# Optimization experiments

Measured on AMD Instinct MI355X. Metric: run time of the kernel, lower is better.

Reference implementation:

```python
import jax, jax.numpy as jnp
import numpy as np

B, N, NODE, EDGE, H, SK, SV, PK, PV = 1, 512, 256, 128, 8, 16, 16, 4, 4
EPS = 1e-8
SCALAR_SCALE = (3 * SK) ** -0.5          # num_attn_logits=3
POINT_SCALE = (3 * PK * (9.0 / 2.0)) ** -0.5
PAIR_SCALE = 3 ** -0.5


def setup_inputs() -> dict:
    key = jax.random.key(0)
    ks = jax.random.split(key, 16)
    s = 0.02
    return {
        "node": jax.random.normal(ks[0], (B, N, NODE), jnp.float32),
        "edge": jax.random.normal(ks[1], (B, N, N, EDGE), jnp.float32),
        "rotations": jax.random.normal(ks[2], (B, N, 3, 3), jnp.float32),
        "translations": jax.random.normal(ks[3], (B, N, 3), jnp.float32),
        "W_sq": jax.random.normal(ks[4], (NODE, H * SK), jnp.float32) * s,
        "W_sk": jax.random.normal(ks[5], (NODE, H * SK), jnp.float32) * s,
        "W_sv": jax.random.normal(ks[6], (NODE, H * SV), jnp.float32) * s,
        "W_pq": jax.random.normal(ks[7], (NODE, H * PK * 3), jnp.float32) * s,
        "W_pk": jax.random.normal(ks[8], (NODE, H * PK * 3), jnp.float32) * s,
        "W_pv": jax.random.normal(ks[9], (NODE, H * PV * 3), jnp.float32) * s,
        "point_weights": jnp.log(jnp.expm1(jnp.ones((H,), jnp.float32))),  # softplus^-1(1)
        "W_pb": jax.random.normal(ks[10], (EDGE, H), jnp.float32) * s,
        "b_pb": jnp.zeros((H,), jnp.float32),
        "W_out": jax.random.normal(ks[11], (H * (SV + EDGE + PV * 4), NODE), jnp.float32) * s,
        "b_out": jnp.zeros((NODE,), jnp.float32),
    }


def reference(node, edge, rotations, translations, W_sq, W_sk, W_sv, W_pq, W_pk, W_pv,
              point_weights, W_pb, b_pb, W_out, b_out):
    b, n, _ = node.shape
    # scalar q/k/v: (b, n, h, d)
    qs = (node @ W_sq).reshape(b, n, H, SK)
    ks_ = (node @ W_sk).reshape(b, n, H, SK)
    vs = (node @ W_sv).reshape(b, n, H, SV)
    # point q/k/v in local frame: (b, n, h, d, 3) -> rotate + translate into global frame
    t = translations[:, :, None, None, :]  # (b, n, 1, 1, 3)
    qp = jnp.einsum('bnhdc,bnrc->bnhdr', (node @ W_pq).reshape(b, n, H, PK, 3), rotations) + t
    kp = jnp.einsum('bnhdc,bnrc->bnhdr', (node @ W_pk).reshape(b, n, H, PK, 3), rotations) + t
    vp = jnp.einsum('bnhdc,bnrc->bnhdr', (node @ W_pv).reshape(b, n, H, PV, 3), rotations) + t

    # scalar logits (b, h, i, j)
    logits_scalar = jnp.einsum('bihd,bjhd->bhij', qs, ks_) * SCALAR_SCALE
    # pairwise bias (b, h, i, j)
    logits_pair = (jnp.einsum('bijd,dh->bhij', edge, W_pb) + b_pb[None, :, None, None]) * PAIR_SCALE
    # point logits: sum_{d,c} ||q - k||^2 via expansion (avoids (b,i,j,h,d,3) tensor)
    q2 = (qp ** 2).sum((-2, -1)).transpose(0, 2, 1)  # (b, h, i)
    k2 = (kp ** 2).sum((-2, -1)).transpose(0, 2, 1)  # (b, h, j)
    cross = jnp.einsum('bihdc,bjhdc->bhij', qp, kp)
    point_dist = q2[:, :, :, None] + k2[:, :, None, :] - 2.0 * cross  # (b, h, i, j)
    pw = jax.nn.softplus(point_weights)[None, :, None, None]  # (1, h, 1, 1)
    logits_points = -0.5 * (point_dist * pw * POINT_SCALE)

    attn = jax.nn.softmax(logits_scalar + logits_points + logits_pair, axis=-1)  # (b, h, i, j)

    res_scalar = jnp.einsum('bhij,bjhd->bihd', attn, vs).reshape(b, n, H * SV)
    res_pair = jnp.einsum('bhij,bijd->bihd', attn, edge).reshape(b, n, H * EDGE)
    res_pts = jnp.einsum('bhij,bjhdr->bihdr', attn, vp) - t  # back to origin
    res_pts = jnp.einsum('bnhdr,bnrc->bnhdc', res_pts, rotations)  # inverse rotation (R^T)
    res_norm = jnp.sqrt((res_pts ** 2).sum(-1) + EPS)  # (b, n, h, d)

    out = jnp.concatenate([
        res_scalar,
        res_pts.reshape(b, n, H * PV * 3),
        res_norm.reshape(b, n, H * PV),
        res_pair,
    ], axis=-1)
    return out @ W_out + b_out
```

## Files before the change

kernel.cpp:

```cpp
#include <hip/hip_runtime.h>
#include <hip/hip_fp16.h>
#include <math.h>

#define NN 512
#define NODE_D 256
#define EDGE_D 128
#define HN 8

#define SCALAR_SCALE 0.14433756729740643f
#define POINT_SCALE  0.13608276348795434f
#define PAIR_SCALE   0.5773502691896258f

#define OFF_QS   0
#define OFF_KS   65536
#define OFF_VS   131072
#define OFF_VP   196608
#define OFF_QCAT 245760
#define OFF_KCAT 393216
#define OFF_FEAT 540672
#define OFF_PRAW OFF_FEAT
#define OFF_LG16 1196032
#define OFF_OUTP 2244608
#define OFF_PART 2768896

__global__ __launch_bounds__(256) void k_projgemm(
    const float* __restrict__ node,
    const float* __restrict__ Wsq, const float* __restrict__ Wsk, const float* __restrict__ Wsv,
    const float* __restrict__ Wpq, const float* __restrict__ Wpk, const float* __restrict__ Wpv,
    float* __restrict__ ws)
{
  __shared__ float As[32 * 33];
  __shared__ float Bs[32 * 36];
  const int t = threadIdx.x;
  const int it = blockIdx.x;
  const int ct = blockIdx.y;

  const float* W; int ncol, col0; float* dst; int ldd, dcol0;
  if (ct < 12) {
    int a = ct >> 2;
    W = (a == 0) ? Wsq : (a == 1) ? Wsk : Wsv;
    ncol = 128; col0 = (ct & 3) * 32;
    dst = ws + ((a == 0) ? OFF_QS : (a == 1) ? OFF_KS : OFF_VS);
    ldd = 128; dcol0 = col0;
  } else {
    int p = ct - 12;
    int a = p / 3, cc = p % 3;
    W = (a == 0) ? Wpq : (a == 1) ? Wpk : Wpv;
    ncol = 96; col0 = cc * 32;
    dst = ws + OFF_PRAW;
    ldd = 288; dcol0 = a * 96 + cc * 32;
  }

  const int row = t & 31, cb = (t >> 5) * 4;
  float4 acc = {0.f, 0.f, 0.f, 0.f};

  for (int kt = 0; kt < 8; ++kt) {
    __syncthreads();
    #pragma unroll
    for (int q = 0; q < 4; ++q) {
      int f = t + q * 256; int r = f >> 5, c = f & 31;
      As[r * 33 + c] = node[(size_t)(it * 32 + r) * 256 + kt * 32 + c];
      Bs[r * 36 + c] = W[(size_t)(kt * 32 + r) * ncol + col0 + c];
    }
    __syncthreads();
    #pragma unroll
    for (int k = 0; k < 32; ++k) {
      float a = As[row * 33 + k];
      float4 b = *(const float4*)&Bs[k * 36 + cb];
      acc.x += a * b.x; acc.y += a * b.y; acc.z += a * b.z; acc.w += a * b.w;
    }
  }
  *(float4*)&dst[(size_t)(it * 32 + row) * ldd + dcol0 + cb] = acc;
}

__global__ __launch_bounds__(256) void k_rot2(
    const float* __restrict__ rotm, const float* __restrict__ trans,
    const float* __restrict__ pw_in, const float* __restrict__ bpb,
    float* __restrict__ ws)
{
  __shared__ float p_l[4][288];
  __shared__ float r_l[4][288];
  __shared__ float q2_l[4][8];
  __shared__ float k2_l[4][8];
  __shared__ float pw_l[8];
  __shared__ float bpb_l[8];
  const int t = threadIdx.x;
  const int n0 = blockIdx.x * 4;
  const float* praw = ws + OFF_PRAW;
  const float* qs_g = ws + OFF_QS;
  const float* ks_g = ws + OFF_KS;

  if (t < 8) {
    float x = pw_in[t];
    pw_l[t] = 0.5f * POINT_SCALE * logf(1.0f + expf(x));
    bpb_l[t] = bpb[t];
  }
  for (int idx = t; idx < 1152; idx += 256) {
    int row = idx / 288, rem = idx % 288;
    p_l[row][rem] = praw[(size_t)(n0 + row) * 288 + rem];
  }
  __syncthreads();

  for (int idx = t; idx < 1152; idx += 256) {
    int row = idx / 288, rem = idx % 288;
    int a = rem / 96, col = rem % 96;
    int rr = col % 3;
    int n = n0 + row;
    const float* R = rotm + (size_t)(n * 3 + rr) * 3;
    const float* P = &p_l[row][a * 96 + (col - rr)];
    float val = P[0] * R[0] + P[1] * R[1] + P[2] * R[2] + trans[n * 3 + rr];
    r_l[row][a * 96 + col] = val;
    if (a == 2) (ws + OFF_VP)[(size_t)n * 96 + col] = val;
  }
  __syncthreads();

  if (t < 64) {
    int row = t >> 4, rem = t & 15;
    int which = rem >> 3, h = rem & 7;
    const float* src = &r_l[row][which * 96 + h * 12];
    float s = 0.f;
    #pragma unroll
    for (int m = 0; m < 12; ++m) s += src[m] * src[m];
    if (which == 0) q2_l[row][h] = s; else k2_l[row][h] = s;
  }
  __syncthreads();

  for (int idx = t; idx < 2304; idx += 256) {
    int side = idx >= 1152;
    int per = idx - side * 1152;
    int row = per / 288, s = per % 288;
    int h = s / 36, e = s % 36;
    int n = n0 + row;
    float val;
    if (!side) {
      val = (e < 16) ? qs_g[(size_t)n * 128 + h * 16 + e] * SCALAR_SCALE
          : (e < 28) ? 2.0f * pw_l[h] * r_l[row][h * 12 + (e - 16)]
          : (e == 32) ? -pw_l[h]
          : (e == 33) ? (bpb_l[h] * PAIR_SCALE - pw_l[h] * q2_l[row][h])
          : 0.f;
      (ws + OFF_QCAT)[(size_t)n * 288 + s] = val;
    } else {
      val = (e < 16) ? ks_g[(size_t)n * 128 + h * 16 + e]
          : (e < 28) ? r_l[row][96 + h * 12 + (e - 16)]
          : (e == 32) ? k2_l[row][h]
          : (e == 33) ? 1.f
          : 0.f;
      (ws + OFF_KCAT)[(size_t)n * 288 + s] = val;
    }
  }
}

__global__ __launch_bounds__(256) void k_S(
    const float* __restrict__ ws_c, __half* __restrict__ lg16)
{
  __shared__ float4 Qt[32 * 36];
  __shared__ float4 Kt[32 * 37];
  __shared__ __half lgst[32 * 32 * 8];
  const int t = threadIdx.x;
  const int it = blockIdx.x, jt = blockIdx.y;
  const float* Qc = ws_c + OFF_QCAT;
  const float* Kc = ws_c + OFF_KCAT;
  const int ti = t >> 4, tj = t & 15;

  for (int hg = 0; hg < 2; ++hg) {
    __syncthreads();
    for (int f = t; f < 1152; f += 256) {
      int row = f / 36, c = f % 36;
      Qt[row * 36 + c] = *(const float4*)&Qc[(size_t)(it * 32 + row) * 288 + hg * 144 + c * 4];
      Kt[row * 37 + c] = *(const float4*)&Kc[(size_t)(jt * 32 + row) * 288 + hg * 144 + c * 4];
    }
    __syncthreads();

    float acc[2][2][4];
    #pragma unroll
    for (int a = 0; a < 2; ++a)
      #pragma unroll
      for (int b = 0; b < 2; ++b)
        #pragma unroll
        for (int h = 0; h < 4; ++h) acc[a][b][h] = 0.f;

    for (int c = 0; c < 9; ++c) {
      #pragma unroll
      for (int hh = 0; hh < 4; ++hh) {
        float4 q0 = Qt[(2 * ti + 0) * 36 + hh * 9 + c];
        float4 q1 = Qt[(2 * ti + 1) * 36 + hh * 9 + c];
        float4 k0 = Kt[(2 * tj + 0) * 37 + hh * 9 + c];
        float4 k1 = Kt[(2 * tj + 1) * 37 + hh * 9 + c];
        acc[0][0][hh] += q0.x * k0.x + q0.y * k0.y + q0.z * k0.z + q0.w * k0.w;
        acc[0][1][hh] += q0.x * k1.x + q0.y * k1.y + q0.z * k1.z + q0.w * k1.w;
        acc[1][0][hh] += q1.x * k0.x + q1.y * k0.y + q1.z * k0.z + q1.w * k0.w;
        acc[1][1][hh] += q1.x * k1.x + q1.y * k1.y + q1.z * k1.z + q1.w * k1.w;
      }
    }
    #pragma unroll
    for (int a = 0; a < 2; ++a)
      #pragma unroll
      for (int b = 0; b < 2; ++b)
        #pragma unroll
        for (int hh = 0; hh < 4; ++hh)
          lgst[((2 * ti + a) * 32 + (2 * tj + b)) * 8 + hg * 4 + hh] = __float2half(acc[a][b][hh]);
  }
  __syncthreads();

  for (int f = t; f < 1024; f += 256) {
    int il = f >> 5, jl = f & 31;
    float4 v = *(const float4*)&lgst[(il * 32 + jl) * 8];
    *(float4*)&lg16[((size_t)(it * 32 + il) * 512 + jt * 32 + jl) * 8] = v;
  }
}

__global__ __launch_bounds__(256) void k_attnfused2(
    const float* __restrict__ edge, const float* __restrict__ ws_r,
    const __half* __restrict__ lg16, const float* __restrict__ Wpb,
    float* __restrict__ part)
{
  __shared__ float e_l[2][32][132];
  __shared__ float w_t[8][33];
  __shared__ float lg_t[32][9];
  __shared__ float mh[8], sh[8], resc[8];
  __shared__ float vsp[4 * 128];
  __shared__ float vpp[4 * 96];

  const int t = threadIdx.x;
  const int jc = blockIdx.x;
  const int i  = blockIdx.y;
  const int dq = t & 31, jg = t >> 5;
  const int sub = t & 15;
  const int hv = dq >> 2;
  const int hp = (dq < 24) ? (dq / 3) : 0;

  const float* eb  = edge + ((size_t)i * 512 + jc * 256) * 128;
  const float* vsg = ws_r + OFF_VS + (size_t)jc * 256 * 128;
  const float* vpg = ws_r + OFF_VP + (size_t)jc * 256 * 96;
  const __half* lgb = lg16 + ((size_t)i * 512 + jc * 256) * 8;

  float wv[8][8];
  #pragma unroll
  for (int dd = 0; dd < 8; ++dd)
    #pragma unroll
    for (int h = 0; h < 8; ++h)
      wv[dd][h] = Wpb[(size_t)(sub * 8 + dd) * 8 + h] * PAIR_SCALE;

  if (t < 8) { mh[t] = -1e30f; sh[t] = 0.f; }

  float4 accp[8];
  #pragma unroll
  for (int h = 0; h < 8; ++h) accp[h] = {0.f, 0.f, 0.f, 0.f};
  float4 accv = {0.f, 0.f, 0.f, 0.f};
  float4 accw = {0.f, 0.f, 0.f, 0.f};

  #pragma unroll
  for (int p = 0; p < 4; ++p) {
    int f = p * 256 + t, r = f >> 5, g = f & 31;
    *(float4*)&e_l[0][r][g * 4] = *(const float4*)&eb[(size_t)r * 128 + g * 4];
  }
  __syncthreads();

  int cur = 0;
  for (int tile = 0; tile < 8; ++tile) {
    float4 nxt0, nxt1, nxt2, nxt3;
    if (tile < 7) {
      const float* ebn = eb + (size_t)(tile + 1) * 32 * 128;
      { int f = t;           int r = f >> 5, g = f & 31; nxt0 = *(const float4*)&ebn[(size_t)r * 128 + g * 4]; }
      { int f = 256 + t;     int r = f >> 5, g = f & 31; nxt1 = *(const float4*)&ebn[(size_t)r * 128 + g * 4]; }
      { int f = 512 + t;     int r = f >> 5, g = f & 31; nxt2 = *(const float4*)&ebn[(size_t)r * 128 + g * 4]; }
      { int f = 768 + t;     int r = f >> 5, g = f & 31; nxt3 = *(const float4*)&ebn[(size_t)r * 128 + g * 4]; }
    }

    #pragma unroll
    for (int pass = 0; pass < 2; ++pass) {
      const int jrow = (t >> 4) + pass * 16;
      float p8[8] = {0, 0, 0, 0, 0, 0, 0, 0};
      #pragma unroll
      for (int k = 0; k < 2; ++k) {
        float4 e = *(float4*)&e_l[cur][jrow][(sub * 2 + k) * 4];
        #pragma unroll
        for (int h = 0; h < 8; ++h)
          p8[h] += e.x * wv[k * 4 + 0][h] + e.y * wv[k * 4 + 1][h]
                 + e.z * wv[k * 4 + 2][h] + e.w * wv[k * 4 + 3][h];
      }
      #pragma unroll
      for (int m = 1; m <= 8; m <<= 1)
        #pragma unroll
        for (int h = 0; h < 8; ++h) p8[h] += __shfl_xor(p8[h], m);
      if (sub == 0) {
        #pragma unroll
        for (int h = 0; h < 8; ++h) lg_t[jrow][h] = p8[h];
      }
    }
    __syncthreads();

    {
      const int hS = t >> 5, jS = t & 31;
      float x = lg_t[jS][hS]
              + __half2float(lgb[(size_t)(tile * 32 + jS) * 8 + hS]);
      float mt = x;
      #pragma unroll
      for (int s = 16; s; s >>= 1) mt = fmaxf(mt, __shfl_xor(mt, s));
      float mo = mh[hS];
      float mn = fmaxf(mo, mt);
      float w = __expf(x - mn);
      float sw = w;
      #pragma unroll
      for (int s = 16; s; s >>= 1) sw += __shfl_xor(sw, s);
      w_t[hS][jS] = w;
      if (jS == 0) {
        float r = __expf(mo - mn);
        resc[hS] = r;
        mh[hS] = mn;
        sh[hS] = sh[hS] * r + sw;
      }
    }
    __syncthreads();

    {
      #pragma unroll
      for (int h = 0; h < 8; ++h) {
        float r = resc[h];
        accp[h].x *= r; accp[h].y *= r; accp[h].z *= r; accp[h].w *= r;
      }
      {
        float rv = resc[hv];
        accv.x *= rv; accv.y *= rv; accv.z *= rv; accv.w *= rv;
      }
      if (dq < 24) {
        float rp = resc[hp];
        accw.x *= rp; accw.y *= rp; accw.z *= rp; accw.w *= rp;
      }
      #pragma unroll
      for (int jj = 0; jj < 4; ++jj) {
        const int j = jg * 4 + jj;
        float4 e = *(float4*)&e_l[cur][j][dq * 4];
        float wj[8];
        #pragma unroll
        for (int h = 0; h < 8; ++h) wj[h] = w_t[h][j];
        #pragma unroll
        for (int h = 0; h < 8; ++h) {
          accp[h].x += wj[h] * e.x; accp[h].y += wj[h] * e.y;
          accp[h].z += wj[h] * e.z; accp[h].w += wj[h] * e.w;
        }
        const int gj = tile * 32 + j;
        float4 v = *(const float4*)&vsg[(size_t)gj * 128 + dq * 4];
        float wvv = wj[hv];
        accv.x += wvv * v.x; accv.y += wvv * v.y;
        accv.z += wvv * v.z; accv.w += wvv * v.w;
        if (dq < 24) {
          float4 pv = *(const float4*)&vpg[(size_t)gj * 96 + dq * 4];
          float wpp = wj[hp];
          accw.x += wpp * pv.x; accw.y += wpp * pv.y;
          accw.z += wpp * pv.z; accw.w += wpp * pv.w;
        }
      }
    }
    __syncthreads();

    if (tile < 7) {
      { int f = t;       int r = f >> 5, g = f & 31; *(float4*)&e_l[cur ^ 1][r][g * 4] = nxt0; }
      { int f = 256 + t; int r = f >> 5, g = f & 31; *(float4*)&e_l[cur ^ 1][r][g * 4] = nxt1; }
      { int f = 512 + t; int r = f >> 5, g = f & 31; *(float4*)&e_l[cur ^ 1][r][g * 4] = nxt2; }
      { int f = 768 + t; int r = f >> 5, g = f & 31; *(float4*)&e_l[cur ^ 1][r][g * 4] = nxt3; }
      cur ^= 1;
      __syncthreads();
    }
  }

  #pragma unroll
  for (int h = 0; h < 8; ++h) {
    accp[h].x += __shfl_xor(accp[h].x, 32);
    accp[h].y += __shfl_xor(accp[h].y, 32);
    accp[h].z += __shfl_xor(accp[h].z, 32);
    accp[h].w += __shfl_xor(accp[h].w, 32);
  }
  accv.x += __shfl_xor(accv.x, 32); accv.y += __shfl_xor(accv.y, 32);
  accv.z += __shfl_xor(accv.z, 32); accv.w += __shfl_xor(accv.w, 32);
  accw.x += __shfl_xor(accw.x, 32); accw.y += __shfl_xor(accw.y, 32);
  accw.z += __shfl_xor(accw.z, 32); accw.w += __shfl_xor(accw.w, 32);

  const int wid = t >> 6;
  float* pl = (float*)e_l;
  if ((t & 63) < 32) {
    #pragma unroll
    for (int h = 0; h < 8; ++h)
      *(float4*)&pl[(size_t)(wid * 8 + h) * 132 + dq * 4] = accp[h];
    *(float4*)&vsp[wid * 128 + dq * 4] = accv;
    if (dq < 24) *(float4*)&vpp[wid * 96 + dq * 4] = accw;
  }
  __syncthreads();

  float* pp = part + ((size_t)i * 2 + jc) * 1280;
  if (t < 8) { pp[t] = mh[t]; pp[8 + t] = sh[t]; }
  {
    const int h = t >> 5, d4 = (t & 31) * 4;
    float4 s = {0.f, 0.f, 0.f, 0.f};
    #pragma unroll
    for (int q = 0; q < 4; ++q) {
      float4 v = *(float4*)&pl[(size_t)(q * 8 + h) * 132 + d4];
      s.x += v.x; s.y += v.y; s.z += v.z; s.w += v.w;
    }
    *(float4*)&pp[16 + h * 128 + d4] = s;
  }
  if (t < 128)
    pp[1040 + t] = vsp[t] + vsp[128 + t] + vsp[256 + t] + vsp[384 + t];
  if (t < 96)
    pp[1168 + t] = vpp[t] + vpp[96 + t] + vpp[192 + t] + vpp[288 + t];
}

__global__ __launch_bounds__(256) void k_amerge(
    const float* __restrict__ part, const float* __restrict__ rotm,
    const float* __restrict__ trans, float* __restrict__ feat)
{
  __shared__ float r0s[8], r1s[8], lis[8];
  __shared__ float op_l[96], rp_l[96];
  const int t = threadIdx.x, i = blockIdx.x;
  const float* p0 = part + (size_t)i * 2560;
  const float* p1 = p0 + 1280;

  if (t < 8) {
    float m0 = p0[t], m1 = p1[t];
    float M = fmaxf(m0, m1);
    float r0 = __expf(m0 - M), r1 = __expf(m1 - M);
    float S = p0[8 + t] * r0 + p1[8 + t] * r1;
    r0s[t] = r0; r1s[t] = r1; lis[t] = 1.0f / S;
  }
  __syncthreads();

  float* frow = feat + (size_t)i * 1280;
  {
    const int h = t >> 5, d4 = (t & 31) * 4;
    float4 a = *(const float4*)&p0[16 + h * 128 + d4];
    float4 b = *(const float4*)&p1[16 + h * 128 + d4];
    float r0 = r0s[h], r1 = r1s[h], li = lis[h];
    float4 o;
    o.x = (a.x * r0 + b.x * r1) * li;
    o.y = (a.y * r0 + b.y * r1) * li;
    o.z = (a.z * r0 + b.z * r1) * li;
    o.w = (a.w * r0 + b.w * r1) * li;
    *(float4*)&frow[256 + h * 128 + d4] = o;
  }
  if (t < 128) {
    int h = t >> 4;
    frow[t] = (p0[1040 + t] * r0s[h] + p1[1040 + t] * r1s[h]) * lis[h];
  }
  if (t < 96) {
    int h = t / 12;
    op_l[t] = (p0[1168 + t] * r0s[h] + p1[1168 + t] * r1s[h]) * lis[h]
            - trans[i * 3 + (t % 3)];
  }
  __syncthreads();

  if (t < 96) {
    int c = t % 3, base = t - c;
    const float* R = rotm + (size_t)i * 9;
    float val = op_l[base] * R[c] + op_l[base + 1] * R[3 + c] + op_l[base + 2] * R[6 + c];
    rp_l[t] = val;
    frow[128 + t] = val;
  }
  __syncthreads();
  if (t < 32) {
    float x = rp_l[t * 3], y = rp_l[t * 3 + 1], z = rp_l[t * 3 + 2];
    frow[224 + t] = sqrtf(x * x + y * y + z * z + 1e-8f);
  }
}

__global__ __launch_bounds__(256) void k_outp(
    const float* __restrict__ feat, const float* __restrict__ Wout,
    float* __restrict__ ws)
{
  __shared__ float As[32 * 33];
  __shared__ float Bs[32 * 36];
  const int t = threadIdx.x;
  const int it = blockIdx.x, ot = blockIdx.y, z = blockIdx.z;
  const int row = t & 31, cb = (t >> 5) * 4;
  float4 acc = {0.f, 0.f, 0.f, 0.f};

  for (int kk = 0; kk < 10; ++kk) {
    int kt = z * 10 + kk;
    __syncthreads();
    #pragma unroll
    for (int q = 0; q < 4; ++q) {
      int f = t + q * 256; int r = f >> 5, c = f & 31;
      As[r * 33 + c] = feat[(size_t)(it * 32 + r) * 1280 + kt * 32 + c];
      Bs[r * 36 + c] = Wout[(size_t)(kt * 32 + r) * 256 + ot * 32 + c];
    }
    __syncthreads();
    #pragma unroll
    for (int k = 0; k < 32; ++k) {
      float a = As[row * 33 + k];
      float4 bv = *(const float4*)&Bs[k * 36 + cb];
      acc.x += a * bv.x; acc.y += a * bv.y; acc.z += a * bv.z; acc.w += a * bv.w;
    }
  }
  float* pc = ws + OFF_OUTP + (size_t)z * 131072;
  *(float4*)&pc[(size_t)(it * 32 + row) * 256 + ot * 32 + cb] = acc;
}

__global__ __launch_bounds__(256) void k_outr(
    const float* __restrict__ ws, const float* __restrict__ bout,
    float* __restrict__ out)
{
  const int q = blockIdx.x * 256 + threadIdx.x;
  const float* pc = ws + OFF_OUTP;
  float4 a = *(const float4*)&pc[(size_t)q * 4];
  float4 b = *(const float4*)&pc[(size_t)q * 4 + 131072];
  float4 c = *(const float4*)&pc[(size_t)q * 4 + 262144];
  float4 d = *(const float4*)&pc[(size_t)q * 4 + 393216];
  float4 bias = *(const float4*)&bout[(q & 63) * 4];
  float4 r;
  r.x = a.x + b.x + c.x + d.x + bias.x;
  r.y = a.y + b.y + c.y + d.y + bias.y;
  r.z = a.z + b.z + c.z + d.z + bias.z;
  r.w = a.w + b.w + c.w + d.w + bias.w;
  *(float4*)&out[(size_t)q * 4] = r;
}

extern "C" void kernel_launch(void* const* d_in, const int* in_sizes, int n_in,
                              void* d_out, int out_size, void* d_ws, size_t ws_size,
                              hipStream_t stream) {
  const float* node  = (const float*)d_in[0];
  const float* edge  = (const float*)d_in[1];
  const float* rotm  = (const float*)d_in[2];
  const float* trans = (const float*)d_in[3];
  const float* Wsq   = (const float*)d_in[4];
  const float* Wsk   = (const float*)d_in[5];
  const float* Wsv   = (const float*)d_in[6];
  const float* Wpq   = (const float*)d_in[7];
  const float* Wpk   = (const float*)d_in[8];
  const float* Wpv   = (const float*)d_in[9];
  const float* pw    = (const float*)d_in[10];
  const float* Wpb   = (const float*)d_in[11];
  const float* bpb   = (const float*)d_in[12];
  const float* Wout  = (const float*)d_in[13];
  const float* bout  = (const float*)d_in[14];
  float* ws   = (float*)d_ws;
  float* out  = (float*)d_out;
  float* feat = ws + OFF_FEAT;
  __half* lg16 = (__half*)(ws + OFF_LG16);
  float* part = ws + OFF_PART;

  k_projgemm<<<dim3(16, 21), 256, 0, stream>>>(node, Wsq, Wsk, Wsv, Wpq, Wpk, Wpv, ws);
  k_rot2<<<128, 256, 0, stream>>>(rotm, trans, pw, bpb, ws);
  k_S<<<dim3(16, 16), 256, 0, stream>>>(ws, lg16);
  k_attnfused2<<<dim3(2, 512), 256, 0, stream>>>(edge, ws, lg16, Wpb, part);
  k_amerge<<<512, 256, 0, stream>>>(part, rotm, trans, feat);
  k_outp<<<dim3(16, 8, 4), 256, 0, stream>>>(feat, Wout, ws);
  k_outr<<<128, 256, 0, stream>>>(ws, bout, out);
}
```

Baseline: 128.4 us.

## Use non-draining barriers, half2 shuffle reductions and transposed weight tile in attention

Replaces __syncthreads in the fused attention tile loop with an inline s_waitcnt lgkmcnt(0)+s_barrier sequence that does not wait on outstanding global loads, so the prefetched edge tile loads stay in flight across barriers. The pair-bias partial sums are packed to half2 before the xor-shuffle reduction, which halves the shuffle count but reduces the logits in fp16. The softmax weight tile is transposed so each j reads 8 head weights as two float4 LDS loads, and the lg16 bias load is hoisted to the top of the tile. Launch bounds now request 4 blocks per CU, which may constrain registers.

Measured after the change: 370.7 us. +188.6%, slower.

```diff
diff --git a/kernel.cpp b/kernel.cpp
--- a/kernel.cpp
+++ b/kernel.cpp
@@ -22,6 +22,12 @@
 #define OFF_LG16 1196032
 #define OFF_OUTP 2244608
 #define OFF_PART 2768896
+
+#define BARRIER_NODRAIN() do {                                   \
+  __builtin_amdgcn_sched_barrier(0);                             \
+  asm volatile("s_waitcnt lgkmcnt(0)\n\ts_barrier" ::: "memory");\
+  __builtin_amdgcn_sched_barrier(0);                             \
+} while (0)
 
 __global__ __launch_bounds__(256) void k_projgemm(
     const float* __restrict__ node,
@@ -209,14 +215,20 @@
   }
 }
 
-__global__ __launch_bounds__(256) void k_attnfused2(
+static __device__ inline __half2 shfl_xor_h2(__half2 h, int m) {
+  int v = __builtin_bit_cast(int, h);
+  v = __shfl_xor(v, m);
+  return __builtin_bit_cast(__half2, v);
+}
+
+__global__ __launch_bounds__(256, 4) void k_attnfused2(
     const float* __restrict__ edge, const float* __restrict__ ws_r,
     const __half* __restrict__ lg16, const float* __restrict__ Wpb,
     float* __restrict__ part)
 {
   __shared__ float e_l[2][32][132];
-  __shared__ float w_t[8][33];
-  __shared__ float lg_t[32][9];
+  __shared__ float w_t2[32][8];
+  __shared__ __half2 lg_th[32][5];
   __shared__ float mh[8], sh[8], resc[8];
   __shared__ float vsp[4 * 128];
   __shared__ float vpp[4 * 96];
@@ -258,13 +270,14 @@
 
   int cur = 0;
   for (int tile = 0; tile < 8; ++tile) {
+    __half lgh = lgb[(size_t)(tile * 32 + (t & 31)) * 8 + (t >> 5)];
     float4 nxt0, nxt1, nxt2, nxt3;
     if (tile < 7) {
       const float* ebn = eb + (size_t)(tile + 1) * 32 * 128;
-      { int f = t;           int r = f >> 5, g = f & 31; nxt0 = *(const float4*)&ebn[(size_t)r * 128 + g * 4]; }
-      { int f = 256 + t;     int r = f >> 5, g = f & 31; nxt1 = *(const float4*)&ebn[(size_t)r * 128 + g * 4]; }
-      { int f = 512 + t;     int r = f >> 5, g = f & 31; nxt2 = *(const float4*)&ebn[(size_t)r * 128 + g * 4]; }
-      { int f = 768 + t;     int r = f >> 5, g = f & 31; nxt3 = *(const float4*)&ebn[(size_t)r * 128 + g * 4]; }
+      { int f = t;       int r = f >> 5, g = f & 31; nxt0 = *(const float4*)&ebn[(size_t)r * 128 + g * 4]; }
+      { int f = 256 + t; int r = f >> 5, g = f & 31; nxt1 = *(const float4*)&ebn[(size_t)r * 128 + g * 4]; }
+      { int f = 512 + t; int r = f >> 5, g = f & 31; nxt2 = *(const float4*)&ebn[(size_t)r * 128 + g * 4]; }
+      { int f = 768 + t; int r = f >> 5, g = f & 31; nxt3 = *(const float4*)&ebn[(size_t)r * 128 + g * 4]; }
     }
 
     #pragma unroll
@@ -279,21 +292,29 @@
           p8[h] += e.x * wv[k * 4 + 0][h] + e.y * wv[k * 4 + 1][h]
                  + e.z * wv[k * 4 + 2][h] + e.w * wv[k * 4 + 3][h];
       }
-      #pragma unroll
-      for (int m = 1; m <= 8; m <<= 1)
-        #pragma unroll
-        for (int h = 0; h < 8; ++h) p8[h] += __shfl_xor(p8[h], m);
+      __half2 h0 = __floats2half2_rn(p8[0], p8[1]);
+      __half2 h1 = __floats2half2_rn(p8[2], p8[3]);
+      __half2 h2 = __floats2half2_rn(p8[4], p8[5]);
+      __half2 h3 = __floats2half2_rn(p8[6], p8[7]);
+      #pragma unroll
+      for (int m = 1; m <= 8; m <<= 1) {
+        h0 = __hadd2(h0, shfl_xor_h2(h0, m));
+        h1 = __hadd2(h1, shfl_xor_h2(h1, m));
+        h2 = __hadd2(h2, shfl_xor_h2(h2, m));
+        h3 = __hadd2(h3, shfl_xor_h2(h3, m));
+      }
       if (sub == 0) {
-        #pragma unroll
-        for (int h = 0; h < 8; ++h) lg_t[jrow][h] = p8[h];
-      }
-    }
-    __syncthreads();
+        lg_th[jrow][0] = h0; lg_th[jrow][1] = h1;
+        lg_th[jrow][2] = h2; lg_th[jrow][3] = h3;
+      }
+    }
+    BARRIER_NODRAIN();
 
     {
       const int hS = t >> 5, jS = t & 31;
-      float x = lg_t[jS][hS]
-              + __half2float(lgb[(size_t)(tile * 32 + jS) * 8 + hS]);
+      __half2 ph = lg_th[jS][hS >> 1];
+      float pv = (hS & 1) ? __high2float(ph) : __low2float(ph);
+      float x = pv + __half2float(lgh);
       float mt = x;
       #pragma unroll
       for (int s = 16; s; s >>= 1) mt = fmaxf(mt, __shfl_xor(mt, s));
@@ -303,7 +324,7 @@
       float sw = w;
       #pragma unroll
       for (int s = 16; s; s >>= 1) sw += __shfl_xor(sw, s);
-      w_t[hS][jS] = w;
+      w_t2[jS][hS] = w;
       if (jS == 0) {
         float r = __expf(mo - mn);
         resc[hS] = r;
@@ -311,7 +332,7 @@
         sh[hS] = sh[hS] * r + sw;
       }
     }
-    __syncthreads();
+    BARRIER_NODRAIN();
 
     {
       #pragma unroll
@@ -331,28 +352,31 @@
       for (int jj = 0; jj < 4; ++jj) {
         const int j = jg * 4 + jj;
         float4 e = *(float4*)&e_l[cur][j][dq * 4];
-        float wj[8];
-        #pragma unroll
-        for (int h = 0; h < 8; ++h) wj[h] = w_t[h][j];
-        #pragma unroll
-        for (int h = 0; h < 8; ++h) {
-          accp[h].x += wj[h] * e.x; accp[h].y += wj[h] * e.y;
-          accp[h].z += wj[h] * e.z; accp[h].w += wj[h] * e.w;
-        }
+        float4 wlo = *(float4*)&w_t2[j][0];
+        float4 whi = *(float4*)&w_t2[j][4];
+        accp[0].x += wlo.x * e.x; accp[0].y += wlo.x * e.y; accp[0].z += wlo.x * e.z; accp[0].w += wlo.x * e.w;
+        accp[1].x += wlo.y * e.x; accp[1].y += wlo.y * e.y; accp[1].z += wlo.y * e.z; accp[1].w += wlo.y * e.w;
+        accp[2].x += wlo.z * e.x; accp[2].y += wlo.z * e.y; accp[2].z += wlo.z * e.z; accp[2].w += wlo.z * e.w;
+        accp[3].x += wlo.w * e.x; accp[3].y += wlo.w * e.y; accp[3].z += wlo.w * e.z; accp[3].w += wlo.w * e.w;
+        accp[4].x += whi.x * e.x; accp[4].y += whi.x * e.y; accp[4].z += whi.x * e.z; accp[4].w += whi.x * e.w;
+        accp[5].x += whi.y * e.x; accp[5].y += whi.y * e.y; accp[5].z += whi.y * e.z; accp[5].w += whi.y * e.w;
+        accp[6].x += whi.z * e.x; accp[6].y += whi.z * e.y; accp[6].z += whi.z * e.z; accp[6].w += whi.z * e.w;
+        accp[7].x += whi.w * e.x; accp[7].y += whi.w * e.y; accp[7].z += whi.w * e.z; accp[7].w += whi.w * e.w;
+
         const int gj = tile * 32 + j;
         float4 v = *(const float4*)&vsg[(size_t)gj * 128 + dq * 4];
-        float wvv = wj[hv];
+        float wvv = w_t2[j][hv];
         accv.x += wvv * v.x; accv.y += wvv * v.y;
         accv.z += wvv * v.z; accv.w += wvv * v.w;
         if (dq < 24) {
-          float4 pv = *(const float4*)&vpg[(size_t)gj * 96 + dq * 4];
-          float wpp = wj[hp];
-          accw.x += wpp * pv.x; accw.y += wpp * pv.y;
-          accw.z += wpp * pv.z; accw.w += wpp * pv.w;
+          float4 pv4 = *(const float4*)&vpg[(size_t)gj * 96 + dq * 4];
+          float wpp = w_t2[j][hp];
+          accw.x += wpp * pv4.x; accw.y += wpp * pv4.y;
+          accw.z += wpp * pv4.z; accw.w += wpp * pv4.w;
         }
       }
     }
-    __syncthreads();
+    BARRIER_NODRAIN();
 
     if (tile < 7) {
       { int f = t;       int r = f >> 5, g = f & 31; *(float4*)&e_l[cur ^ 1][r][g * 4] = nxt0; }
@@ -360,7 +384,7 @@
       { int f = 512 + t; int r = f >> 5, g = f & 31; *(float4*)&e_l[cur ^ 1][r][g * 4] = nxt2; }
       { int f = 768 + t; int r = f >> 5, g = f & 31; *(float4*)&e_l[cur ^ 1][r][g * 4] = nxt3; }
       cur ^= 1;
-      __syncthreads();
+      BARRIER_NODRAIN();
     }
   }
 
@@ -375,6 +399,8 @@
   accv.z += __shfl_xor(accv.z, 32); accv.w += __shfl_xor(accv.w, 32);
   accw.x += __shfl_xor(accw.x, 32); accw.y += __shfl_xor(accw.y, 32);
   accw.z += __shfl_xor(accw.z, 32); accw.w += __shfl_xor(accw.w, 32);
+
+  __syncthreads();
 
   const int wid = t >> 6;
   float* pl = (float*)e_l;
```
